# Kernel tuning notes

Measured on AMD Instinct MI355X. Metric: run time of the kernel, lower is better.

## Reference

```python
import jax, jax.numpy as jnp
import numpy as np

# dims
B, T, H = 4, 2048, 768
HEADS, D = 4, 768          # GATConv(out_channels=768, heads=4, concat=False)
L = 3                      # num_layers
WIN = 2
K = 2 * WIN + 1
EPS = 1e-5
NEG_SLOPE = 0.2            # PyG GATConv leaky_relu slope


def setup_inputs() -> dict:
    key = jax.random.key(0)
    ks = jax.random.split(key, 4)
    s = 1.0 / np.sqrt(H)
    x = jax.random.normal(ks[0], (B, T, H), jnp.float32)
    W = jax.random.normal(ks[1], (L, H, HEADS, D), jnp.float32) * s   # lin weights per layer
    a_src = jax.random.normal(ks[2], (L, HEADS, D), jnp.float32) * s  # att_src
    a_dst = jax.random.normal(ks[3], (L, HEADS, D), jnp.float32) * s  # att_dst
    bias = jnp.zeros((L, D), jnp.float32)                             # GATConv bias (concat=False -> [D])
    gamma = jnp.ones((L, H), jnp.float32)                             # LayerNorm weight
    beta = jnp.zeros((L, H), jnp.float32)                             # LayerNorm bias
    return {"x": x, "W": W, "a_src": a_src, "a_dst": a_dst,
            "bias": bias, "gamma": gamma, "beta": beta}


def _layernorm(z, g, b):
    m = jnp.mean(z, axis=-1, keepdims=True)
    v = jnp.mean((z - m) ** 2, axis=-1, keepdims=True)
    return (z - m) * jax.lax.rsqrt(v + EPS) * g + b


def _gat_layer(x, Wl, asrc_w, adst_w, bias_l, idx, mask):
    # x: [B,T,H]; banded GAT with neighborhoods idx: [T,K] (clipped), mask: [T,K]
    h = jnp.einsum('bti,ihd->bthd', x, Wl)                 # [B,T,heads,D]
    asrc = jnp.einsum('bthd,hd->bth', h, asrc_w)           # per-source-node score term
    adst = jnp.einsum('bthd,hd->bth', h, adst_w)           # per-target-node score term
    h_nb = h[:, idx]                                       # [B,T,K,heads,D] gathered neighbors j
    score = jax.nn.leaky_relu(asrc[:, idx] + adst[:, :, None, :], NEG_SLOPE)  # [B,T,K,heads]
    score = jnp.where(mask[None, :, :, None], score, -jnp.inf)
    attn = jax.nn.softmax(score, axis=2)                   # softmax over incoming edges per target
    out = jnp.einsum('btkh,btkhd->bthd', attn, h_nb)       # weighted aggregation
    return out.mean(axis=2) + bias_l                       # concat=False -> mean over heads


def reference(x, W, a_src, a_dst, bias, gamma, beta):
    # banded neighborhood indices (window edges both directions + self-loop from PyG default)
    offs = jnp.arange(-WIN, WIN + 1)
    idx = jnp.arange(T)[:, None] + offs[None, :]           # [T,K]
    mask = (idx >= 0) & (idx < T)
    idx = jnp.clip(idx, 0, T - 1)
    for l in range(L):
        res = x
        y = _gat_layer(x, W[l], a_src[l], a_dst[l], bias[l], idx, mask)
        x = _layernorm(y + res, gamma[l], beta[l])         # dropout = identity in eval
    return x
```

## Files before the change

kernel.cpp:

```cpp
#include <hip/hip_runtime.h>
#include <stdint.h>

#define TT 2048
#define BB 4
#define HH 768
#define NHEADS 4
#define DD 768
#define NN 3072
#define LL 3
#define BT 8192
#define KNB 5
#define NBLK 12
#define TPB 4
#define NROWS 8

typedef __bf16 bf16x8 __attribute__((ext_vector_type(8)));
typedef float f32x4 __attribute__((ext_vector_type(4)));

__device__ __forceinline__ unsigned short f2bf(float f){
  union { float f; unsigned u; } v; v.f = f;
  unsigned u = v.u;
  return (unsigned short)((u + 0x7FFFu + ((u >> 16) & 1u)) >> 16);
}
__device__ __forceinline__ float bf2f(unsigned short h){
  union { unsigned u; float f; } v; v.u = ((unsigned)h) << 16;
  return v.f;
}
__device__ __forceinline__ void gload16(const unsigned short* g, unsigned short* l){
  __builtin_amdgcn_global_load_lds((const __attribute__((address_space(1))) void*)g,
                                   (__attribute__((address_space(3))) void*)l, 16, 0, 0);
}

__global__ void wt_kernel(const float* __restrict__ W, unsigned short* __restrict__ Wt){
  __shared__ float tile[32][33];
  int l = blockIdx.z;
  int n0 = blockIdx.x * 32, k0 = blockIdx.y * 32;
  int tx = threadIdx.x, ty = threadIdx.y;
  const float* Wl = W + (size_t)l * HH * NN;
  for (int r = 0; r < 4; r++)
    tile[ty + r*8][tx] = Wl[(size_t)(k0 + ty + r*8) * NN + n0 + tx];
  __syncthreads();
  unsigned short* Wtl = Wt + (size_t)l * NN * HH;
  for (int r = 0; r < 4; r++){
    int n = n0 + ty + r*8;
    Wtl[(size_t)n * HH + k0 + tx] = f2bf(tile[tx][ty + r*8]);
  }
}

__global__ void xconv_kernel(const float* __restrict__ x, unsigned short* __restrict__ xb){
  int i = blockIdx.x * blockDim.x + threadIdx.x;
  float4 v = ((const float4*)x)[i];
  ushort4 o;
  o.x = f2bf(v.x); o.y = f2bf(v.y); o.z = f2bf(v.z); o.w = f2bf(v.w);
  *(ushort4*)(xb + (size_t)i * 4) = o;
}

#define BM 128
#define BN 128
#define BK 32

__global__ __launch_bounds__(256, 2) void gemm_kernel(
    const unsigned short* __restrict__ xb,
    const unsigned short* __restrict__ wt,
    unsigned short* __restrict__ hout,
    const float* __restrict__ a_srcl,
    const float* __restrict__ a_dstl,
    float* __restrict__ psrc,
    float* __restrict__ pdst){
  __shared__ __align__(16) unsigned short xs[BM][32];
  __shared__ __align__(16) unsigned short wsd[BN][32];
  int bm = blockIdx.y * BM;
  int bn = blockIdx.x * BN;
  int tid = threadIdx.x;
  int wave = tid >> 6, lane = tid & 63;
  int m16 = lane & 15, q = lane >> 4;
  int wm = (wave >> 1) * 64, wn = (wave & 1) * 64;
  int rA = wave * 32 + (lane >> 2);
  int cc = (lane & 3) ^ ((lane >> 3) & 3);
  const unsigned short* ga0 = xb + (size_t)(bm + rA) * HH + cc * 8;
  const unsigned short* ga1 = ga0 + (size_t)16 * HH;
  const unsigned short* gb0 = wt + (size_t)(bn + rA) * HH + cc * 8;
  const unsigned short* gb1 = gb0 + (size_t)16 * HH;
  unsigned short* la0 = &xs[wave * 32][0];
  unsigned short* la1 = &xs[wave * 32 + 16][0];
  unsigned short* lb0 = &wsd[wave * 32][0];
  unsigned short* lb1 = &wsd[wave * 32 + 16][0];
  int sw = (m16 >> 1) & 3;
  int rdcol = (q ^ sw) * 8;
  f32x4 acc[4][4] = {};
  for (int k0 = 0; k0 < HH; k0 += BK){
    gload16(ga0 + k0, la0);
    gload16(ga1 + k0, la1);
    gload16(gb0 + k0, lb0);
    gload16(gb1 + k0, lb1);
    __syncthreads();
    bf16x8 af[4], bfr[4];
    for (int i = 0; i < 4; i++)
      af[i] = __builtin_bit_cast(bf16x8, *(const uint4*)(&xs[wm + i*16 + m16][rdcol]));
    for (int j = 0; j < 4; j++)
      bfr[j] = __builtin_bit_cast(bf16x8, *(const uint4*)(&wsd[wn + j*16 + m16][rdcol]));
    for (int i = 0; i < 4; i++)
      for (int j = 0; j < 4; j++)
        acc[i][j] = __builtin_amdgcn_mfma_f32_16x16x32_bf16(af[i], bfr[j], acc[i][j], 0, 0, 0);
    __syncthreads();
  }
  for (int i = 0; i < 4; i++){
    int row0 = bm + wm + i*16 + q*4;
    for (int j = 0; j < 4; j++){
      int col = bn + wn + j*16 + m16;
      unsigned short* hp = hout + (size_t)row0 * NN + col;
      hp[0]            = f2bf(acc[i][j][0]);
      hp[NN]           = f2bf(acc[i][j][1]);
      hp[2*(size_t)NN] = f2bf(acc[i][j][2]);
      hp[3*(size_t)NN] = f2bf(acc[i][j][3]);
    }
  }
  int col0 = bn + wn;
  int head = col0 / DD;
  int blk  = (col0 % DD) >> 6;
  float wsrc[4], wdstw[4];
  for (int j = 0; j < 4; j++){
    int n = col0 + j*16 + m16;
    wsrc[j]  = a_srcl[n];
    wdstw[j] = a_dstl[n];
  }
  for (int i = 0; i < 4; i++){
    for (int reg = 0; reg < 4; reg++){
      float ss = 0.f, dd = 0.f;
      for (int j = 0; j < 4; j++){
        float v = acc[i][j][reg];
        ss += v * wsrc[j];
        dd += v * wdstw[j];
      }
      ss += __shfl_xor(ss, 1, 64); dd += __shfl_xor(dd, 1, 64);
      ss += __shfl_xor(ss, 2, 64); dd += __shfl_xor(dd, 2, 64);
      ss += __shfl_xor(ss, 4, 64); dd += __shfl_xor(dd, 4, 64);
      ss += __shfl_xor(ss, 8, 64); dd += __shfl_xor(dd, 8, 64);
      if (m16 == 0){
        int row = bm + wm + i*16 + q*4 + reg;
        size_t slot = (size_t)row * (NHEADS * NBLK) + head * NBLK + blk;
        psrc[slot] = ss;
        pdst[slot] = dd;
      }
    }
  }
}

__global__ __launch_bounds__(256) void srcred_kernel(
    const float* __restrict__ psrc, const float* __restrict__ pdst,
    float* __restrict__ asrc, float* __restrict__ adst){
  int task = blockIdx.x * 256 + threadIdx.x;
  const float* ps = psrc + (size_t)task * NBLK;
  const float* pd = pdst + (size_t)task * NBLK;
  float ss = 0.f, dd = 0.f;
  for (int i = 0; i < NBLK; i++){ ss += ps[i]; dd += pd[i]; }
  asrc[task] = ss;
  adst[task] = dd;
}

__global__ __launch_bounds__(256) void attn_ln_kernel(const unsigned short* __restrict__ h,
    const float* __restrict__ asrc, const float* __restrict__ adst,
    const float* __restrict__ x_in, const float* __restrict__ bias_l,
    const float* __restrict__ gamma_l, const float* __restrict__ beta_l,
    float* __restrict__ x_out, unsigned short* __restrict__ xb_next){
  int bid = blockIdx.x;
  int grp = ((bid & 7) << 8) | (bid >> 3);
  int token0 = grp * TPB;
  int t0 = token0 & (TT - 1);
  int bseq = token0 >> 11;
  int tid = threadIdx.x;
  int wave = tid >> 6, lane = tid & 63;
  __shared__ __align__(16) unsigned short hs[NROWS][NN];
  __shared__ float attn_s[TPB][NHEADS][KNB];
  __shared__ float rs[4][TPB], rq[4][TPB];
  for (int it = 0; it < 12; it++){
    int idx = it * 256 + tid;
    int j = idx / (NN/8);
    int c = idx % (NN/8);
    int g = t0 - 2 + j;
    g = min(max(g, 0), TT - 1);
    const unsigned short* src = h + ((size_t)(bseq * TT + g)) * NN + c * 8;
    gload16(src, ((unsigned short*)hs) + (size_t)(it * 256 + wave * 64) * 8);
  }
  if (tid < TPB * NHEADS){
    int ti = tid >> 2, head = tid & 3;
    int token = token0 + ti, t = t0 + ti;
    float sc[KNB];
    float mx = -3.0e38f;
    float ad = adst[token * NHEADS + head];
    for (int k = 0; k < KNB; k++){
      int tn = t + k - 2;
      if (tn >= 0 && tn < TT){
        float s = asrc[(token + k - 2) * NHEADS + head] + ad;
        s = s > 0.f ? s : 0.2f * s;
        sc[k] = s; mx = fmaxf(mx, s);
      } else sc[k] = -3.0e38f;
    }
    float den = 0.f;
    for (int k = 0; k < KNB; k++){
      float e = (sc[k] > -1.0e38f) ? __expf(sc[k] - mx) : 0.f;
      sc[k] = e; den += e;
    }
    float inv = 0.25f / den;
    for (int k = 0; k < KNB; k++) attn_s[ti][head][k] = sc[k] * inv;
  }
  __syncthreads();
  float y[3][TPB] = {};
  for (int hd = 0; hd < NHEADS; hd++){
    float ac[TPB][KNB];
    for (int ti = 0; ti < TPB; ti++)
      for (int k = 0; k < KNB; k++) ac[ti][k] = attn_s[ti][hd][k];
    for (int r = 0; r < 3; r++){
      int d = hd * DD + tid + r * 256;
      for (int j = 0; j < NROWS; j++){
        float v = bf2f(hs[j][d]);
        #pragma unroll
        for (int ti = 0; ti < TPB; ti++){
          int k = j - ti;
          if (k >= 0 && k < KNB) y[r][ti] += ac[ti][k] * v;
        }
      }
    }
  }
  float sum[TPB] = {}, sq[TPB] = {};
  for (int r = 0; r < 3; r++){
    int d = tid + r * 256;
    float bl = bias_l[d];
    for (int ti = 0; ti < TPB; ti++){
      float zz = y[r][ti] + bl + x_in[(size_t)(token0 + ti) * HH + d];
      y[r][ti] = zz; sum[ti] += zz; sq[ti] += zz * zz;
    }
  }
  for (int off = 32; off > 0; off >>= 1){
    for (int ti = 0; ti < TPB; ti++){
      sum[ti] += __shfl_xor(sum[ti], off, 64);
      sq[ti]  += __shfl_xor(sq[ti], off, 64);
    }
  }
  if (lane == 0)
    for (int ti = 0; ti < TPB; ti++){ rs[wave][ti] = sum[ti]; rq[wave][ti] = sq[ti]; }
  __syncthreads();
  for (int ti = 0; ti < TPB; ti++){
    float ts = rs[0][ti] + rs[1][ti] + rs[2][ti] + rs[3][ti];
    float tq = rq[0][ti] + rq[1][ti] + rq[2][ti] + rq[3][ti];
    float mean = ts * (1.f / HH);
    float var = tq * (1.f / HH) - mean * mean;
    float rstd = rsqrtf(var + 1e-5f);
    for (int r = 0; r < 3; r++){
      int d = tid + r * 256;
      float o = (y[r][ti] - mean) * rstd * gamma_l[d] + beta_l[d];
      x_out[(size_t)(token0 + ti) * HH + d] = o;
      xb_next[(size_t)(token0 + ti) * HH + d] = f2bf(o);
    }
  }
}

extern "C" void kernel_launch(void* const* d_in, const int* in_sizes, int n_in,
                              void* d_out, int out_size, void* d_ws, size_t ws_size,
                              hipStream_t stream) {
  const float* x     = (const float*)d_in[0];
  const float* W     = (const float*)d_in[1];
  const float* a_src = (const float*)d_in[2];
  const float* a_dst = (const float*)d_in[3];
  const float* bias  = (const float*)d_in[4];
  const float* gamma = (const float*)d_in[5];
  const float* beta  = (const float*)d_in[6];
  float* out = (float*)d_out;

  char* ws = (char*)d_ws;
  size_t off = 0;
  auto alloc = [&](size_t bytes)->char*{
    char* p = ws + off;
    off = (off + bytes + 255) & ~(size_t)255;
    return p;
  };
  unsigned short* wt   = (unsigned short*)alloc((size_t)LL * NN * HH * 2);
  unsigned short* xb   = (unsigned short*)alloc((size_t)BT * HH * 2);
  unsigned short* hbuf = (unsigned short*)alloc((size_t)BT * NN * 2);
  float* psrc  = (float*)alloc((size_t)BT * NHEADS * NBLK * 4);
  float* pdst  = (float*)alloc((size_t)BT * NHEADS * NBLK * 4);
  float* asrcb = (float*)alloc((size_t)BT * NHEADS * 4);
  float* adstb = (float*)alloc((size_t)BT * NHEADS * 4);

  wt_kernel<<<dim3(NN/32, HH/32, LL), dim3(32, 8), 0, stream>>>(W, wt);
  xconv_kernel<<<(BT * HH / 4) / 256, 256, 0, stream>>>(x, xb);

  for (int l = 0; l < LL; l++){
    const float* xin = (l == 0) ? x : out;
    gemm_kernel<<<dim3(NN / BN, BT / BM), 256, 0, stream>>>(
        xb, wt + (size_t)l * NN * HH, hbuf,
        a_src + (size_t)l * NHEADS * DD, a_dst + (size_t)l * NHEADS * DD,
        psrc, pdst);
    srcred_kernel<<<BT * NHEADS / 256, 256, 0, stream>>>(psrc, pdst, asrcb, adstb);
    attn_ln_kernel<<<BT / TPB, 256, 0, stream>>>(hbuf, asrcb, adstb, xin,
        bias + (size_t)l * DD, gamma + (size_t)l * HH, beta + (size_t)l * HH,
        out, xb);
  }
}
```

Baseline: 374.0 us.

## Double GEMM K-tile and vectorize attention/LayerNorm kernel with 384 threads

The GEMM K-tile goes from 32 to 64 with a new XOR swizzle over 8 column groups. This halves the number of barrier-separated load iterations and runs two MFMA rounds per tile. The attention+LayerNorm kernel now uses 384 threads, each owning 8 contiguous features of one token. That allows 16-byte LDS reads of the bf16 rows, float4 global loads and stores, and a per-token reduction through shared partials. The cost is higher register use and a changed LDS swizzle pattern, which could add bank conflicts if it is wrong.

```diff
diff --git a/kernel.cpp b/kernel.cpp
--- a/kernel.cpp
+++ b/kernel.cpp
@@ -11,7 +11,7 @@
 #define BT 8192
 #define KNB 5
 #define NBLK 12
-#define TPB 4
+#define ATPB 4
 #define NROWS 8
 
 typedef __bf16 bf16x8 __attribute__((ext_vector_type(8)));
@@ -57,7 +57,7 @@
 
 #define BM 128
 #define BN 128
-#define BK 32
+#define BK 64
 
 __global__ __launch_bounds__(256, 2) void gemm_kernel(
     const unsigned short* __restrict__ xb,
@@ -67,38 +67,48 @@
     const float* __restrict__ a_dstl,
     float* __restrict__ psrc,
     float* __restrict__ pdst){
-  __shared__ __align__(16) unsigned short xs[BM][32];
-  __shared__ __align__(16) unsigned short wsd[BN][32];
+  __shared__ __align__(16) unsigned short xs[BM][BK];
+  __shared__ __align__(16) unsigned short wsd[BN][BK];
   int bm = blockIdx.y * BM;
   int bn = blockIdx.x * BN;
   int tid = threadIdx.x;
   int wave = tid >> 6, lane = tid & 63;
   int m16 = lane & 15, q = lane >> 4;
   int wm = (wave >> 1) * 64, wn = (wave & 1) * 64;
-  int rA = wave * 32 + (lane >> 2);
-  int cc = (lane & 3) ^ ((lane >> 3) & 3);
-  const unsigned short* ga0 = xb + (size_t)(bm + rA) * HH + cc * 8;
-  const unsigned short* ga1 = ga0 + (size_t)16 * HH;
-  const unsigned short* gb0 = wt + (size_t)(bn + rA) * HH + cc * 8;
-  const unsigned short* gb1 = gb0 + (size_t)16 * HH;
-  unsigned short* la0 = &xs[wave * 32][0];
-  unsigned short* la1 = &xs[wave * 32 + 16][0];
-  unsigned short* lb0 = &wsd[wave * 32][0];
-  unsigned short* lb1 = &wsd[wave * 32 + 16][0];
-  int sw = (m16 >> 1) & 3;
-  int rdcol = (q ^ sw) * 8;
+  int r8 = lane >> 3, c8 = lane & 7;
+  int cg = (c8 ^ r8) * 8;
+  const unsigned short* ga[4]; const unsigned short* gb[4];
+  unsigned short* la[4]; unsigned short* lb[4];
+  #pragma unroll
+  for (int s = 0; s < 4; s++){
+    int row = wave * 32 + s * 8;
+    ga[s] = xb + (size_t)(bm + row + r8) * HH + cg;
+    gb[s] = wt + (size_t)(bn + row + r8) * HH + cg;
+    la[s] = &xs[row][0];
+    lb[s] = &wsd[row][0];
+  }
+  int rd0 = ((0 + q) ^ (m16 & 7)) * 8;
+  int rd1 = ((4 + q) ^ (m16 & 7)) * 8;
   f32x4 acc[4][4] = {};
   for (int k0 = 0; k0 < HH; k0 += BK){
-    gload16(ga0 + k0, la0);
-    gload16(ga1 + k0, la1);
-    gload16(gb0 + k0, lb0);
-    gload16(gb1 + k0, lb1);
+    #pragma unroll
+    for (int s = 0; s < 4; s++){
+      gload16(ga[s] + k0, la[s]);
+      gload16(gb[s] + k0, lb[s]);
+    }
     __syncthreads();
     bf16x8 af[4], bfr[4];
     for (int i = 0; i < 4; i++)
-      af[i] = __builtin_bit_cast(bf16x8, *(const uint4*)(&xs[wm + i*16 + m16][rdcol]));
+      af[i] = __builtin_bit_cast(bf16x8, *(const uint4*)(&xs[wm + i*16 + m16][rd0]));
     for (int j = 0; j < 4; j++)
-      bfr[j] = __builtin_bit_cast(bf16x8, *(const uint4*)(&wsd[wn + j*16 + m16][rdcol]));
+      bfr[j] = __builtin_bit_cast(bf16x8, *(const uint4*)(&wsd[wn + j*16 + m16][rd0]));
+    for (int i = 0; i < 4; i++)
+      for (int j = 0; j < 4; j++)
+        acc[i][j] = __builtin_amdgcn_mfma_f32_16x16x32_bf16(af[i], bfr[j], acc[i][j], 0, 0, 0);
+    for (int i = 0; i < 4; i++)
+      af[i] = __builtin_bit_cast(bf16x8, *(const uint4*)(&xs[wm + i*16 + m16][rd1]));
+    for (int j = 0; j < 4; j++)
+      bfr[j] = __builtin_bit_cast(bf16x8, *(const uint4*)(&wsd[wn + j*16 + m16][rd1]));
     for (int i = 0; i < 4; i++)
       for (int j = 0; j < 4; j++)
         acc[i][j] = __builtin_amdgcn_mfma_f32_16x16x32_bf16(af[i], bfr[j], acc[i][j], 0, 0, 0);
@@ -158,31 +168,30 @@
   adst[task] = dd;
 }
 
-__global__ __launch_bounds__(256) void attn_ln_kernel(const unsigned short* __restrict__ h,
+__global__ __launch_bounds__(384) void attn_ln_kernel(const unsigned short* __restrict__ h,
     const float* __restrict__ asrc, const float* __restrict__ adst,
     const float* __restrict__ x_in, const float* __restrict__ bias_l,
     const float* __restrict__ gamma_l, const float* __restrict__ beta_l,
     float* __restrict__ x_out, unsigned short* __restrict__ xb_next){
   int bid = blockIdx.x;
   int grp = ((bid & 7) << 8) | (bid >> 3);
-  int token0 = grp * TPB;
+  int token0 = grp * ATPB;
   int t0 = token0 & (TT - 1);
   int bseq = token0 >> 11;
   int tid = threadIdx.x;
   int wave = tid >> 6, lane = tid & 63;
   __shared__ __align__(16) unsigned short hs[NROWS][NN];
-  __shared__ float attn_s[TPB][NHEADS][KNB];
-  __shared__ float rs[4][TPB], rq[4][TPB];
-  for (int it = 0; it < 12; it++){
-    int idx = it * 256 + tid;
-    int j = idx / (NN/8);
-    int c = idx % (NN/8);
+  __shared__ float attn_s[ATPB][NHEADS][KNB];
+  __shared__ float part_s[ATPB * 96], part_q[ATPB * 96];
+  __shared__ float mv_mean[ATPB], mv_rstd[ATPB];
+  #pragma unroll
+  for (int j = 0; j < NROWS; j++){
     int g = t0 - 2 + j;
     g = min(max(g, 0), TT - 1);
-    const unsigned short* src = h + ((size_t)(bseq * TT + g)) * NN + c * 8;
-    gload16(src, ((unsigned short*)hs) + (size_t)(it * 256 + wave * 64) * 8);
-  }
-  if (tid < TPB * NHEADS){
+    const unsigned short* src = h + ((size_t)(bseq * TT + g)) * NN + tid * 8;
+    gload16(src, &hs[j][wave * 512]);
+  }
+  if (tid < ATPB * NHEADS){
     int ti = tid >> 2, head = tid & 3;
     int token = token0 + ti, t = t0 + ti;
     float sc[KNB];
@@ -205,54 +214,70 @@
     for (int k = 0; k < KNB; k++) attn_s[ti][head][k] = sc[k] * inv;
   }
   __syncthreads();
-  float y[3][TPB] = {};
+  int ti = tid / 96, c = tid % 96;
+  int token = token0 + ti;
+  float ac[NHEADS][KNB];
+  for (int hd = 0; hd < NHEADS; hd++)
+    for (int k = 0; k < KNB; k++) ac[hd][k] = attn_s[ti][hd][k];
+  float y8[8] = {};
   for (int hd = 0; hd < NHEADS; hd++){
-    float ac[TPB][KNB];
-    for (int ti = 0; ti < TPB; ti++)
-      for (int k = 0; k < KNB; k++) ac[ti][k] = attn_s[ti][hd][k];
-    for (int r = 0; r < 3; r++){
-      int d = hd * DD + tid + r * 256;
-      for (int j = 0; j < NROWS; j++){
-        float v = bf2f(hs[j][d]);
-        #pragma unroll
-        for (int ti = 0; ti < TPB; ti++){
-          int k = j - ti;
-          if (k >= 0 && k < KNB) y[r][ti] += ac[ti][k] * v;
-        }
-      }
-    }
-  }
-  float sum[TPB] = {}, sq[TPB] = {};
-  for (int r = 0; r < 3; r++){
-    int d = tid + r * 256;
-    float bl = bias_l[d];
-    for (int ti = 0; ti < TPB; ti++){
-      float zz = y[r][ti] + bl + x_in[(size_t)(token0 + ti) * HH + d];
-      y[r][ti] = zz; sum[ti] += zz; sq[ti] += zz * zz;
-    }
-  }
-  for (int off = 32; off > 0; off >>= 1){
-    for (int ti = 0; ti < TPB; ti++){
-      sum[ti] += __shfl_xor(sum[ti], off, 64);
-      sq[ti]  += __shfl_xor(sq[ti], off, 64);
-    }
-  }
-  if (lane == 0)
-    for (int ti = 0; ti < TPB; ti++){ rs[wave][ti] = sum[ti]; rq[wave][ti] = sq[ti]; }
+    #pragma unroll
+    for (int k = 0; k < KNB; k++){
+      bf16x8 v = __builtin_bit_cast(bf16x8, *(const uint4*)(&hs[ti + k][hd * DD + c * 8]));
+      float a = ac[hd][k];
+      #pragma unroll
+      for (int e = 0; e < 8; e++) y8[e] += a * (float)v[e];
+    }
+  }
+  float xr[8], bb[8];
+  { const float4* p = (const float4*)&x_in[(size_t)token * HH + c * 8];
+    *(float4*)&xr[0] = p[0]; *(float4*)&xr[4] = p[1]; }
+  { const float4* p = (const float4*)&bias_l[c * 8];
+    *(float4*)&bb[0] = p[0]; *(float4*)&bb[4] = p[1]; }
+  float s = 0.f, sq = 0.f;
+  #pragma unroll
+  for (int e = 0; e < 8; e++){
+    float zz = y8[e] + bb[e] + xr[e];
+    y8[e] = zz; s += zz; sq += zz * zz;
+  }
+  part_s[tid] = s; part_q[tid] = sq;
   __syncthreads();
-  for (int ti = 0; ti < TPB; ti++){
-    float ts = rs[0][ti] + rs[1][ti] + rs[2][ti] + rs[3][ti];
-    float tq = rq[0][ti] + rq[1][ti] + rq[2][ti] + rq[3][ti];
-    float mean = ts * (1.f / HH);
-    float var = tq * (1.f / HH) - mean * mean;
-    float rstd = rsqrtf(var + 1e-5f);
-    for (int r = 0; r < 3; r++){
-      int d = tid + r * 256;
-      float o = (y[r][ti] - mean) * rstd * gamma_l[d] + beta_l[d];
-      x_out[(size_t)(token0 + ti) * HH + d] = o;
-      xb_next[(size_t)(token0 + ti) * HH + d] = f2bf(o);
-    }
-  }
+  if (wave < ATPB){
+    float vs = part_s[wave * 96 + lane];
+    float vq = part_q[wave * 96 + lane];
+    if (lane < 32){
+      vs += part_s[wave * 96 + 64 + lane];
+      vq += part_q[wave * 96 + 64 + lane];
+    }
+    for (int off = 32; off > 0; off >>= 1){
+      vs += __shfl_xor(vs, off, 64);
+      vq += __shfl_xor(vq, off, 64);
+    }
+    if (lane == 0){
+      float mean = vs * (1.f / HH);
+      float var = vq * (1.f / HH) - mean * mean;
+      mv_mean[wave] = mean;
+      mv_rstd[wave] = rsqrtf(var + 1e-5f);
+    }
+  }
+  __syncthreads();
+  float mean = mv_mean[ti], rstd = mv_rstd[ti];
+  float gr[8], br[8];
+  { const float4* p = (const float4*)&gamma_l[c * 8];
+    *(float4*)&gr[0] = p[0]; *(float4*)&gr[4] = p[1]; }
+  { const float4* p = (const float4*)&beta_l[c * 8];
+    *(float4*)&br[0] = p[0]; *(float4*)&br[4] = p[1]; }
+  float o[8];
+  unsigned short o16[8];
+  #pragma unroll
+  for (int e = 0; e < 8; e++){
+    o[e] = (y8[e] - mean) * rstd * gr[e] + br[e];
+    o16[e] = f2bf(o[e]);
+  }
+  float* xo = &x_out[(size_t)token * HH + c * 8];
+  *(float4*)&xo[0] = *(float4*)&o[0];
+  *(float4*)&xo[4] = *(float4*)&o[4];
+  *(uint4*)(&xb_next[(size_t)token * HH + c * 8]) = *(uint4*)&o16[0];
 }
 
 extern "C" void kernel_launch(void* const* d_in, const int* in_sizes, int n_in,
@@ -292,7 +317,7 @@
         a_src + (size_t)l * NHEADS * DD, a_dst + (size_t)l * NHEADS * DD,
         psrc, pdst);
     srcred_kernel<<<BT * NHEADS / 256, 256, 0, stream>>>(psrc, pdst, asrcb, adstb);
-    attn_ln_kernel<<<BT / TPB, 256, 0, stream>>>(hbuf, asrcb, adstb, xin,
+    attn_ln_kernel<<<BT / ATPB, 384, 0, stream>>>(hbuf, asrcb, adstb, xin,
         bias + (size_t)l * DD, gamma + (size_t)l * HH, beta + (size_t)l * HH,
         out, xb);
   }
```

Result: faster. 340.1 us (-9.1%).
